# Kernel tuning notes

Measured on AMD Instinct MI355X. Metric: run time of the kernel, lower is better.

The kernel has to match this reference:

```python
import jax, jax.numpy as jnp
import numpy as np

P = 4            # capsule pose side
D = P * P        # capsule dim = 16
N_CLASSES = 10
N_ROUT = 3


def squash(s, axis=-1):
    sq = (s ** 2).sum(axis=axis, keepdims=True)
    scale = sq / (1.0 + sq)
    return scale * s / jnp.sqrt(sq)


def setup_inputs() -> dict:
    key = jax.random.key(0)
    k1, k2, k3 = jax.random.split(key, 3)
    N, C, W, H = 32, 32, 16, 16
    l = jax.random.normal(k1, (N, C, D, W, H), dtype=jnp.float32)
    g = jax.random.normal(k2, (N, N_CLASSES, D), dtype=jnp.float32)
    weight = jax.random.normal(k3, (1, C, 1, N_CLASSES, P, P), dtype=jnp.float32)
    return {"l": l, "g": g, "weight": weight}


def reference(l, g, weight):
    N, C, Dd, W, H = l.shape
    K = N_CLASSES
    # (N, C, D, W, H) -> (N, C, W*H, P, P)
    lr = jnp.transpose(l, (0, 1, 3, 4, 2)).reshape(N, C, W * H, P, P)
    w = weight.reshape(C, K, P, P)
    # votes: broadcasted small matmul over (N, C, WH, K)
    V = jnp.einsum('ncwij,ckjl->ncwkil', lr, w)          # (N, C, WH, K, P, P)
    V = V.reshape(N, 1, 1, C * W * H, K, Dd)             # (N,1,1,B,K,D)
    gb = g[:, None, None, None, :, :]                    # (N,1,1,1,K,D)
    b = (gb * V).sum(axis=-1, keepdims=True)             # (N,1,1,B,K,1)
    # dynamic routing, iters = N_ROUT
    for i in range(N_ROUT):
        c = jax.nn.softmax(b, axis=4)
        v = squash((c * V).sum(axis=3, keepdims=True))   # (N,1,1,1,K,D)
        if i != N_ROUT - 1:
            b = b + (V * v).sum(axis=-1, keepdims=True)
    a = jax.nn.sigmoid(jnp.linalg.norm(v, axis=-1))      # (N,1,1,1,K)
    v = v.reshape(N, K, Dd)
    a = a.reshape(N, K)
    return (a, v)
```

## Files before the change

### kernel.cpp

```cpp
#include <hip/hip_runtime.h>
#include <math.h>

#define NB 32
#define CB 32
#define KC 10
#define PAD_LRT 260
#define PAD_TP  168


__device__ __forceinline__ float squash_term(const float* __restrict__ sp, int n, int tid) {
    const float* p = sp + (size_t)n * (CB * 160) + tid;
    float t0 = 0.f, t1 = 0.f, t2 = 0.f, t3 = 0.f;
    #pragma unroll
    for (int cc = 0; cc < 32; cc += 4) {
        t0 += p[cc * 160];       t1 += p[(cc + 1) * 160];
        t2 += p[(cc + 2) * 160]; t3 += p[(cc + 3) * 160];
    }
    float ssum = (t0 + t1) + (t2 + t3);
    float sq = ssum * ssum;
    sq += __shfl_xor(sq, 1, 16);
    sq += __shfl_xor(sq, 2, 16);
    sq += __shfl_xor(sq, 4, 16);
    sq += __shfl_xor(sq, 8, 16);
    sq = fmaxf(sq, 1e-30f);
    return ssum * sq / ((1.f + sq) * sqrtf(sq));
}

__device__ __forceinline__ void softmax_c(const float lr[16], const float* __restrict__ E,
                                          float* __restrict__ c_out, int tid) {
    float b[KC];
    #pragma unroll
    for (int k = 0; k < KC; ++k) {
        const float4* e4 = (const float4*)(E + k * 16);
        float4 e0 = e4[0], e1 = e4[1], e2 = e4[2], e3 = e4[3];
        float acc = 0.f;
        acc = fmaf(lr[0], e0.x, acc);  acc = fmaf(lr[1], e0.y, acc);
        acc = fmaf(lr[2], e0.z, acc);  acc = fmaf(lr[3], e0.w, acc);
        acc = fmaf(lr[4], e1.x, acc);  acc = fmaf(lr[5], e1.y, acc);
        acc = fmaf(lr[6], e1.z, acc);  acc = fmaf(lr[7], e1.w, acc);
        acc = fmaf(lr[8], e2.x, acc);  acc = fmaf(lr[9], e2.y, acc);
        acc = fmaf(lr[10], e2.z, acc); acc = fmaf(lr[11], e2.w, acc);
        acc = fmaf(lr[12], e3.x, acc); acc = fmaf(lr[13], e3.y, acc);
        acc = fmaf(lr[14], e3.z, acc); acc = fmaf(lr[15], e3.w, acc);
        b[k] = acc;
    }
    float mx = b[0];
    #pragma unroll
    for (int k = 1; k < KC; ++k) mx = fmaxf(mx, b[k]);
    float sum = 0.f;
    #pragma unroll
    for (int k = 0; k < KC; ++k) { b[k] = __expf(b[k] - mx); sum += b[k]; }
    const float inv = 1.f / sum;
    #pragma unroll
    for (int k = 0; k < KC; ++k) c_out[k * 256 + tid] = b[k] * inv;
}

__device__ __forceinline__ void tp_stage(const float* __restrict__ lrTp,
                                         const float* __restrict__ cl,
                                         float* __restrict__ Tp, int tid) {
    const int mg  = tid >> 4;
    const int r   = tid & 15;
    const int ija = r & 7;
    const int ijb = ija + 8;
    const int k0  = (r >> 3) * 5;
    const float4* lp0 = (const float4*)(lrTp + ija * PAD_LRT + mg * 16);
    const float4* lp1 = (const float4*)(lrTp + ijb * PAD_LRT + mg * 16);
    float4 a0 = lp0[0], a1 = lp0[1], a2 = lp0[2], a3 = lp0[3];
    float4 b0 = lp1[0], b1 = lp1[1], b2 = lp1[2], b3 = lp1[3];
    #pragma unroll
    for (int kk = 0; kk < 5; ++kk) {
        const int k = k0 + kk;
        const float4* cp = (const float4*)(cl + k * 256 + mg * 16);
        float4 c0 = cp[0], c1 = cp[1], c2 = cp[2], c3 = cp[3];
        float t0 = 0.f, t1 = 0.f;
        t0 = fmaf(c0.x, a0.x, t0); t1 = fmaf(c0.x, b0.x, t1);
        t0 = fmaf(c0.y, a0.y, t0); t1 = fmaf(c0.y, b0.y, t1);
        t0 = fmaf(c0.z, a0.z, t0); t1 = fmaf(c0.z, b0.z, t1);
        t0 = fmaf(c0.w, a0.w, t0); t1 = fmaf(c0.w, b0.w, t1);
        t0 = fmaf(c1.x, a1.x, t0); t1 = fmaf(c1.x, b1.x, t1);
        t0 = fmaf(c1.y, a1.y, t0); t1 = fmaf(c1.y, b1.y, t1);
        t0 = fmaf(c1.z, a1.z, t0); t1 = fmaf(c1.z, b1.z, t1);
        t0 = fmaf(c1.w, a1.w, t0); t1 = fmaf(c1.w, b1.w, t1);
        t0 = fmaf(c2.x, a2.x, t0); t1 = fmaf(c2.x, b2.x, t1);
        t0 = fmaf(c2.y, a2.y, t0); t1 = fmaf(c2.y, b2.y, t1);
        t0 = fmaf(c2.z, a2.z, t0); t1 = fmaf(c2.z, b2.z, t1);
        t0 = fmaf(c2.w, a2.w, t0); t1 = fmaf(c2.w, b2.w, t1);
        t0 = fmaf(c3.x, a3.x, t0); t1 = fmaf(c3.x, b3.x, t1);
        t0 = fmaf(c3.y, a3.y, t0); t1 = fmaf(c3.y, b3.y, t1);
        t0 = fmaf(c3.z, a3.z, t0); t1 = fmaf(c3.z, b3.z, t1);
        t0 = fmaf(c3.w, a3.w, t0); t1 = fmaf(c3.w, b3.w, t1);
        Tp[mg * PAD_TP + k * 16 + ija] = t0;
        Tp[mg * PAD_TP + k * 16 + ijb] = t1;
    }
}

__device__ __forceinline__ void t_reduce(const float* __restrict__ Tp,
                                         float* __restrict__ T, int tid) {
    if (tid < 160) {
        float t = 0.f;
        #pragma unroll
        for (int mg = 0; mg < 16; ++mg) t += Tp[mg * PAD_TP + tid];
        T[tid] = t;
    }
}

__device__ __forceinline__ void s_write(const float* __restrict__ T,
                                        const float* __restrict__ w,
                                        float* __restrict__ s_base, int tid) {
    if (tid < 160) {
        const int k = tid >> 4;
        const int i = (tid >> 2) & 3;
        const int le = tid & 3;
        const float4 t4 = *(const float4*)(T + k * 16 + i * 4);
        float sv = 0.f;
        sv = fmaf(t4.x, w[k * 16 + 0 + le], sv);
        sv = fmaf(t4.y, w[k * 16 + 4 + le], sv);
        sv = fmaf(t4.z, w[k * 16 + 8 + le], sv);
        sv = fmaf(t4.w, w[k * 16 + 12 + le], sv);
        s_base[tid] = sv;
    }
}

__global__ __launch_bounds__(256) void caps_main(
    const float* __restrict__ l, const float* __restrict__ g,
    const float* __restrict__ weight,
    const float* __restrict__ sp0, const float* __restrict__ sp1,
    float* __restrict__ s_out, int nv)
{
    __shared__ __align__(16) float w_lds[160];
    __shared__ __align__(16) float aeff_lds[160];
    __shared__ __align__(16) float E_lds[160];
    __shared__ __align__(16) float lrT[16 * PAD_LRT];
    __shared__ __align__(16) float c_lds[KC * 256];
    __shared__ __align__(16) float Tp[16 * PAD_TP];
    __shared__ __align__(16) float T_lds[160];

    const int tid = threadIdx.x;
    const int n = blockIdx.x >> 5;
    const int c = blockIdx.x & 31;

    if (tid < 160) w_lds[tid] = weight[c * 160 + tid];

    float lr[16];
    const float* lbase = l + (size_t)(n * CB + c) * 4096 + tid;
    #pragma unroll
    for (int ij = 0; ij < 16; ++ij) lr[ij] = lbase[ij * 256];
    #pragma unroll
    for (int ij = 0; ij < 16; ++ij) lrT[ij * PAD_LRT + tid] = lr[ij];

    if (tid < 160) {
        float a = g[n * 160 + tid];
        if (nv > 0) a += squash_term(sp0, n, tid);
        if (nv > 1) a += squash_term(sp1, n, tid);
        aeff_lds[tid] = a;
    }
    __syncthreads();

    if (tid < 160) {
        const int k = tid >> 4, i = (tid >> 2) & 3, j = tid & 3;
        const float4 a4 = *(const float4*)(aeff_lds + k * 16 + i * 4);
        const float4 w4 = *(const float4*)(w_lds + k * 16 + j * 4);
        E_lds[tid] = a4.x * w4.x + a4.y * w4.y + a4.z * w4.z + a4.w * w4.w;
    }
    __syncthreads();

    softmax_c(lr, E_lds, c_lds, tid);
    __syncthreads();
    tp_stage(lrT, c_lds, Tp, tid);
    __syncthreads();
    t_reduce(Tp, T_lds, tid);
    __syncthreads();
    s_write(T_lds, w_lds, s_out + (size_t)blockIdx.x * 160, tid);
}

__global__ __launch_bounds__(256) void caps_final(
    const float* __restrict__ sp2, float* __restrict__ out)
{
    const int idx = blockIdx.x * 256 + threadIdx.x;
    const int nk = idx >> 4;
    const int d = idx & 15;
    const int n = nk / 10;
    const int k = nk - n * 10;
    const float* sp = sp2 + (size_t)n * (CB * 160) + k * 16 + d;
    float t0 = 0.f, t1 = 0.f, t2 = 0.f, t3 = 0.f;
    #pragma unroll
    for (int cc = 0; cc < 32; cc += 4) {
        t0 += sp[cc * 160];       t1 += sp[(cc + 1) * 160];
        t2 += sp[(cc + 2) * 160]; t3 += sp[(cc + 3) * 160];
    }
    float ssum = (t0 + t1) + (t2 + t3);
    float sq = ssum * ssum;
    sq += __shfl_xor(sq, 1, 16);
    sq += __shfl_xor(sq, 2, 16);
    sq += __shfl_xor(sq, 4, 16);
    sq += __shfl_xor(sq, 8, 16);
    sq = fmaxf(sq, 1e-30f);
    out[320 + nk * 16 + d] = ssum * sq / ((1.f + sq) * sqrtf(sq));
    if (d == 0) {
        const float nrm = sq / (1.f + sq);
        out[nk] = 1.f / (1.f + __expf(-nrm));
    }
}

extern "C" void kernel_launch(void* const* d_in, const int* in_sizes, int n_in,
                              void* d_out, int out_size, void* d_ws, size_t ws_size,
                              hipStream_t stream) {
    const float* l = (const float*)d_in[0];
    const float* g = (const float*)d_in[1];
    const float* w = (const float*)d_in[2];
    float* out = (float*)d_out;
    float* ws = (float*)d_ws;

    float* s0 = ws;
    float* s1 = ws + 163840;
    float* s2 = ws + 327680;

    caps_main<<<dim3(NB * CB), dim3(256), 0, stream>>>(l, g, w, nullptr, nullptr, s0, 0);
    caps_main<<<dim3(NB * CB), dim3(256), 0, stream>>>(l, g, w, s0, nullptr, s1, 1);
    caps_main<<<dim3(NB * CB), dim3(256), 0, stream>>>(l, g, w, s0, s1, s2, 2);
    caps_final<<<dim3(20), dim3(256), 0, stream>>>(s2, out);
}
```

Baseline: 29.12 us.

## Fuse final squash into last routing pass via atomics and last-block counter

Removes the separate caps_final launch. In the last routing pass each block atomically adds its partial s into a per-sample sum, and a per-sample counter picks the last finishing block, which then computes squash and the sigmoid activation. The sum buffer and counters are zeroed inside the second pass. The global load of l is also moved after the g/squash prologue to overlap the two. This saves one launch and the 32-way reduction read, at the cost of atomic contention and a non-deterministic summation order.

```diff
diff --git a/kernel.cpp b/kernel.cpp
--- a/kernel.cpp
+++ b/kernel.cpp
@@ -104,28 +104,15 @@
     }
 }
 
-__device__ __forceinline__ void s_write(const float* __restrict__ T,
-                                        const float* __restrict__ w,
-                                        float* __restrict__ s_base, int tid) {
-    if (tid < 160) {
-        const int k = tid >> 4;
-        const int i = (tid >> 2) & 3;
-        const int le = tid & 3;
-        const float4 t4 = *(const float4*)(T + k * 16 + i * 4);
-        float sv = 0.f;
-        sv = fmaf(t4.x, w[k * 16 + 0 + le], sv);
-        sv = fmaf(t4.y, w[k * 16 + 4 + le], sv);
-        sv = fmaf(t4.z, w[k * 16 + 8 + le], sv);
-        sv = fmaf(t4.w, w[k * 16 + 12 + le], sv);
-        s_base[tid] = sv;
-    }
-}
-
 __global__ __launch_bounds__(256) void caps_main(
     const float* __restrict__ l, const float* __restrict__ g,
     const float* __restrict__ weight,
     const float* __restrict__ sp0, const float* __restrict__ sp1,
-    float* __restrict__ s_out, int nv)
+    float* __restrict__ s_out,
+    float* __restrict__ s2_sum,
+    int* __restrict__ ctr,
+    float* __restrict__ out,
+    int nv)
 {
     __shared__ __align__(16) float w_lds[160];
     __shared__ __align__(16) float aeff_lds[160];
@@ -134,19 +121,19 @@
     __shared__ __align__(16) float c_lds[KC * 256];
     __shared__ __align__(16) float Tp[16 * PAD_TP];
     __shared__ __align__(16) float T_lds[160];
+    __shared__ int lastflag;
 
     const int tid = threadIdx.x;
-    const int n = blockIdx.x >> 5;
-    const int c = blockIdx.x & 31;
+    const int bid = blockIdx.x;
+    const int n = bid >> 5;
+    const int c = bid & 31;
+
+    if (nv == 1) {
+        if (bid < 20) s2_sum[bid * 256 + tid] = 0.f;
+        else if (bid == 20 && tid < 32) ctr[tid] = 0;
+    }
 
     if (tid < 160) w_lds[tid] = weight[c * 160 + tid];
-
-    float lr[16];
-    const float* lbase = l + (size_t)(n * CB + c) * 4096 + tid;
-    #pragma unroll
-    for (int ij = 0; ij < 16; ++ij) lr[ij] = lbase[ij * 256];
-    #pragma unroll
-    for (int ij = 0; ij < 16; ++ij) lrT[ij * PAD_LRT + tid] = lr[ij];
 
     if (tid < 160) {
         float a = g[n * 160 + tid];
@@ -154,6 +141,13 @@
         if (nv > 1) a += squash_term(sp1, n, tid);
         aeff_lds[tid] = a;
     }
+
+    float lr[16];
+    const float* lbase = l + (size_t)bid * 4096 + tid;
+    #pragma unroll
+    for (int ij = 0; ij < 16; ++ij) lr[ij] = lbase[ij * 256];
+    #pragma unroll
+    for (int ij = 0; ij < 16; ++ij) lrT[ij * PAD_LRT + tid] = lr[ij];
     __syncthreads();
 
     if (tid < 160) {
@@ -170,35 +164,49 @@
     __syncthreads();
     t_reduce(Tp, T_lds, tid);
     __syncthreads();
-    s_write(T_lds, w_lds, s_out + (size_t)blockIdx.x * 160, tid);
-}
-
-__global__ __launch_bounds__(256) void caps_final(
-    const float* __restrict__ sp2, float* __restrict__ out)
-{
-    const int idx = blockIdx.x * 256 + threadIdx.x;
-    const int nk = idx >> 4;
-    const int d = idx & 15;
-    const int n = nk / 10;
-    const int k = nk - n * 10;
-    const float* sp = sp2 + (size_t)n * (CB * 160) + k * 16 + d;
-    float t0 = 0.f, t1 = 0.f, t2 = 0.f, t3 = 0.f;
-    #pragma unroll
-    for (int cc = 0; cc < 32; cc += 4) {
-        t0 += sp[cc * 160];       t1 += sp[(cc + 1) * 160];
-        t2 += sp[(cc + 2) * 160]; t3 += sp[(cc + 3) * 160];
-    }
-    float ssum = (t0 + t1) + (t2 + t3);
-    float sq = ssum * ssum;
-    sq += __shfl_xor(sq, 1, 16);
-    sq += __shfl_xor(sq, 2, 16);
-    sq += __shfl_xor(sq, 4, 16);
-    sq += __shfl_xor(sq, 8, 16);
-    sq = fmaxf(sq, 1e-30f);
-    out[320 + nk * 16 + d] = ssum * sq / ((1.f + sq) * sqrtf(sq));
-    if (d == 0) {
-        const float nrm = sq / (1.f + sq);
-        out[nk] = 1.f / (1.f + __expf(-nrm));
+
+    if (tid < 160) {
+        const int k = tid >> 4;
+        const int i = (tid >> 2) & 3;
+        const int le = tid & 3;
+        const float4 t4 = *(const float4*)(T_lds + k * 16 + i * 4);
+        float sv = 0.f;
+        sv = fmaf(t4.x, w_lds[k * 16 + 0 + le], sv);
+        sv = fmaf(t4.y, w_lds[k * 16 + 4 + le], sv);
+        sv = fmaf(t4.z, w_lds[k * 16 + 8 + le], sv);
+        sv = fmaf(t4.w, w_lds[k * 16 + 12 + le], sv);
+        if (nv < 2) {
+            s_out[(size_t)bid * 160 + tid] = sv;
+        } else {
+            atomicAdd(&s2_sum[n * 160 + tid], sv);
+        }
+    }
+
+    if (nv != 2) return;
+
+    __syncthreads();
+    if (tid == 0) {
+        asm volatile("s_waitcnt vmcnt(0)" ::: "memory");
+        lastflag = (atomicAdd(&ctr[n], 1) == CB - 1);
+    }
+    __syncthreads();
+    if (!lastflag) return;
+
+    if (tid < 160) {
+        const float ssum = __hip_atomic_load(&s2_sum[n * 160 + tid],
+                                             __ATOMIC_RELAXED, __HIP_MEMORY_SCOPE_AGENT);
+        float sq = ssum * ssum;
+        sq += __shfl_xor(sq, 1, 16);
+        sq += __shfl_xor(sq, 2, 16);
+        sq += __shfl_xor(sq, 4, 16);
+        sq += __shfl_xor(sq, 8, 16);
+        sq = fmaxf(sq, 1e-30f);
+        const int k = tid >> 4, d = tid & 15;
+        out[320 + (n * KC + k) * 16 + d] = ssum * sq / ((1.f + sq) * sqrtf(sq));
+        if (d == 0) {
+            const float nrm = sq / (1.f + sq);
+            out[n * KC + k] = 1.f / (1.f + __expf(-nrm));
+        }
     }
 }
 
@@ -211,12 +219,15 @@
     float* out = (float*)d_out;
     float* ws = (float*)d_ws;
 
-    float* s0 = ws;
-    float* s1 = ws + 163840;
-    float* s2 = ws + 327680;
-
-    caps_main<<<dim3(NB * CB), dim3(256), 0, stream>>>(l, g, w, nullptr, nullptr, s0, 0);
-    caps_main<<<dim3(NB * CB), dim3(256), 0, stream>>>(l, g, w, s0, nullptr, s1, 1);
-    caps_main<<<dim3(NB * CB), dim3(256), 0, stream>>>(l, g, w, s0, s1, s2, 2);
-    caps_final<<<dim3(20), dim3(256), 0, stream>>>(s2, out);
-}
+    float* s0     = ws;
+    float* s1     = ws + 163840;
+    float* s2_sum = ws + 327680;
+    int*   ctr    = (int*)(ws + 332800);
+
+    caps_main<<<dim3(NB * CB), dim3(256), 0, stream>>>(
+        l, g, w, nullptr, nullptr, s0, s2_sum, ctr, out, 0);
+    caps_main<<<dim3(NB * CB), dim3(256), 0, stream>>>(
+        l, g, w, s0, nullptr, s1, s2_sum, ctr, out, 1);
+    caps_main<<<dim3(NB * CB), dim3(256), 0, stream>>>(
+        l, g, w, s0, s1, nullptr, s2_sum, ctr, out, 2);
+}
```

After: 35.98 us. +23.5%, slower.

## Double threads per block, split class work across thread pairs, fuse reduction stages

Applied to the files above, without the earlier changes.

Blocks grow from 256 to 512 threads. Each pair of threads shares one spatial position and splits the ten classes, combining the softmax max and sum with a lane shuffle. The two squash-term reductions run in parallel on separate thread groups, and the T reduction is folded into the final weight multiply so one barrier and one shared buffer go away. The aim is more parallelism and shorter per-thread serial chains in a latency-bound kernel. In exchange, every global load of l is issued twice, and more threads per block may reduce how many blocks fit on a CU.

```diff
diff --git a/kernel.cpp b/kernel.cpp
--- a/kernel.cpp
+++ b/kernel.cpp
@@ -8,8 +8,8 @@
 #define PAD_TP  168
 
 
-__device__ __forceinline__ float squash_term(const float* __restrict__ sp, int n, int tid) {
-    const float* p = sp + (size_t)n * (CB * 160) + tid;
+__device__ __forceinline__ float squash_term(const float* __restrict__ sp, int n, int t) {
+    const float* p = sp + (size_t)n * (CB * 160) + t;
     float t0 = 0.f, t1 = 0.f, t2 = 0.f, t3 = 0.f;
     #pragma unroll
     for (int cc = 0; cc < 32; cc += 4) {
@@ -26,151 +26,136 @@
     return ssum * sq / ((1.f + sq) * sqrtf(sq));
 }
 
-__device__ __forceinline__ void softmax_c(const float lr[16], const float* __restrict__ E,
-                                          float* __restrict__ c_out, int tid) {
-    float b[KC];
-    #pragma unroll
-    for (int k = 0; k < KC; ++k) {
-        const float4* e4 = (const float4*)(E + k * 16);
-        float4 e0 = e4[0], e1 = e4[1], e2 = e4[2], e3 = e4[3];
-        float acc = 0.f;
-        acc = fmaf(lr[0], e0.x, acc);  acc = fmaf(lr[1], e0.y, acc);
-        acc = fmaf(lr[2], e0.z, acc);  acc = fmaf(lr[3], e0.w, acc);
-        acc = fmaf(lr[4], e1.x, acc);  acc = fmaf(lr[5], e1.y, acc);
-        acc = fmaf(lr[6], e1.z, acc);  acc = fmaf(lr[7], e1.w, acc);
-        acc = fmaf(lr[8], e2.x, acc);  acc = fmaf(lr[9], e2.y, acc);
-        acc = fmaf(lr[10], e2.z, acc); acc = fmaf(lr[11], e2.w, acc);
-        acc = fmaf(lr[12], e3.x, acc); acc = fmaf(lr[13], e3.y, acc);
-        acc = fmaf(lr[14], e3.z, acc); acc = fmaf(lr[15], e3.w, acc);
-        b[k] = acc;
-    }
-    float mx = b[0];
-    #pragma unroll
-    for (int k = 1; k < KC; ++k) mx = fmaxf(mx, b[k]);
-    float sum = 0.f;
-    #pragma unroll
-    for (int k = 0; k < KC; ++k) { b[k] = __expf(b[k] - mx); sum += b[k]; }
-    const float inv = 1.f / sum;
-    #pragma unroll
-    for (int k = 0; k < KC; ++k) c_out[k * 256 + tid] = b[k] * inv;
-}
-
-__device__ __forceinline__ void tp_stage(const float* __restrict__ lrTp,
-                                         const float* __restrict__ cl,
-                                         float* __restrict__ Tp, int tid) {
-    const int mg  = tid >> 4;
-    const int r   = tid & 15;
-    const int ija = r & 7;
-    const int ijb = ija + 8;
-    const int k0  = (r >> 3) * 5;
-    const float4* lp0 = (const float4*)(lrTp + ija * PAD_LRT + mg * 16);
-    const float4* lp1 = (const float4*)(lrTp + ijb * PAD_LRT + mg * 16);
-    float4 a0 = lp0[0], a1 = lp0[1], a2 = lp0[2], a3 = lp0[3];
-    float4 b0 = lp1[0], b1 = lp1[1], b2 = lp1[2], b3 = lp1[3];
-    #pragma unroll
-    for (int kk = 0; kk < 5; ++kk) {
-        const int k = k0 + kk;
-        const float4* cp = (const float4*)(cl + k * 256 + mg * 16);
-        float4 c0 = cp[0], c1 = cp[1], c2 = cp[2], c3 = cp[3];
-        float t0 = 0.f, t1 = 0.f;
-        t0 = fmaf(c0.x, a0.x, t0); t1 = fmaf(c0.x, b0.x, t1);
-        t0 = fmaf(c0.y, a0.y, t0); t1 = fmaf(c0.y, b0.y, t1);
-        t0 = fmaf(c0.z, a0.z, t0); t1 = fmaf(c0.z, b0.z, t1);
-        t0 = fmaf(c0.w, a0.w, t0); t1 = fmaf(c0.w, b0.w, t1);
-        t0 = fmaf(c1.x, a1.x, t0); t1 = fmaf(c1.x, b1.x, t1);
-        t0 = fmaf(c1.y, a1.y, t0); t1 = fmaf(c1.y, b1.y, t1);
-        t0 = fmaf(c1.z, a1.z, t0); t1 = fmaf(c1.z, b1.z, t1);
-        t0 = fmaf(c1.w, a1.w, t0); t1 = fmaf(c1.w, b1.w, t1);
-        t0 = fmaf(c2.x, a2.x, t0); t1 = fmaf(c2.x, b2.x, t1);
-        t0 = fmaf(c2.y, a2.y, t0); t1 = fmaf(c2.y, b2.y, t1);
-        t0 = fmaf(c2.z, a2.z, t0); t1 = fmaf(c2.z, b2.z, t1);
-        t0 = fmaf(c2.w, a2.w, t0); t1 = fmaf(c2.w, b2.w, t1);
-        t0 = fmaf(c3.x, a3.x, t0); t1 = fmaf(c3.x, b3.x, t1);
-        t0 = fmaf(c3.y, a3.y, t0); t1 = fmaf(c3.y, b3.y, t1);
-        t0 = fmaf(c3.z, a3.z, t0); t1 = fmaf(c3.z, b3.z, t1);
-        t0 = fmaf(c3.w, a3.w, t0); t1 = fmaf(c3.w, b3.w, t1);
-        Tp[mg * PAD_TP + k * 16 + ija] = t0;
-        Tp[mg * PAD_TP + k * 16 + ijb] = t1;
-    }
-}
-
-__device__ __forceinline__ void t_reduce(const float* __restrict__ Tp,
-                                         float* __restrict__ T, int tid) {
-    if (tid < 160) {
-        float t = 0.f;
-        #pragma unroll
-        for (int mg = 0; mg < 16; ++mg) t += Tp[mg * PAD_TP + tid];
-        T[tid] = t;
-    }
-}
-
-__device__ __forceinline__ void s_write(const float* __restrict__ T,
-                                        const float* __restrict__ w,
-                                        float* __restrict__ s_base, int tid) {
-    if (tid < 160) {
-        const int k = tid >> 4;
-        const int i = (tid >> 2) & 3;
-        const int le = tid & 3;
-        const float4 t4 = *(const float4*)(T + k * 16 + i * 4);
-        float sv = 0.f;
-        sv = fmaf(t4.x, w[k * 16 + 0 + le], sv);
-        sv = fmaf(t4.y, w[k * 16 + 4 + le], sv);
-        sv = fmaf(t4.z, w[k * 16 + 8 + le], sv);
-        sv = fmaf(t4.w, w[k * 16 + 12 + le], sv);
-        s_base[tid] = sv;
-    }
-}
-
-__global__ __launch_bounds__(256) void caps_main(
+__global__ __launch_bounds__(512, 8) void caps_main(
     const float* __restrict__ l, const float* __restrict__ g,
     const float* __restrict__ weight,
     const float* __restrict__ sp0, const float* __restrict__ sp1,
     float* __restrict__ s_out, int nv)
 {
     __shared__ __align__(16) float w_lds[160];
-    __shared__ __align__(16) float aeff_lds[160];
+    __shared__ __align__(16) float aeffA[160];
+    __shared__ __align__(16) float aeffB[160];
     __shared__ __align__(16) float E_lds[160];
     __shared__ __align__(16) float lrT[16 * PAD_LRT];
     __shared__ __align__(16) float c_lds[KC * 256];
     __shared__ __align__(16) float Tp[16 * PAD_TP];
-    __shared__ __align__(16) float T_lds[160];
 
     const int tid = threadIdx.x;
-    const int n = blockIdx.x >> 5;
-    const int c = blockIdx.x & 31;
-
-    if (tid < 160) w_lds[tid] = weight[c * 160 + tid];
-
-    float lr[16];
-    const float* lbase = l + (size_t)(n * CB + c) * 4096 + tid;
-    #pragma unroll
-    for (int ij = 0; ij < 16; ++ij) lr[ij] = lbase[ij * 256];
-    #pragma unroll
-    for (int ij = 0; ij < 16; ++ij) lrT[ij * PAD_LRT + tid] = lr[ij];
+    const int bid = blockIdx.x;
+    const int n = bid >> 5;
+    const int c = bid & 31;
 
     if (tid < 160) {
         float a = g[n * 160 + tid];
         if (nv > 0) a += squash_term(sp0, n, tid);
-        if (nv > 1) a += squash_term(sp1, n, tid);
-        aeff_lds[tid] = a;
+        aeffA[tid] = a;
+        w_lds[tid] = weight[c * 160 + tid];
+    } else if (tid >= 256 && tid < 416) {
+        const int t = tid - 256;
+        aeffB[t] = (nv > 1) ? squash_term(sp1, n, t) : 0.f;
+    }
+
+    const int m  = tid >> 1;
+    const int kh = tid & 1;
+    float lr[16];
+    {
+        const float* lbase = l + (size_t)bid * 4096 + m;
+        #pragma unroll
+        for (int ij = 0; ij < 16; ++ij) lr[ij] = lbase[ij * 256];
+        if (kh == 0) {
+            #pragma unroll
+            for (int ij = 0; ij < 16; ++ij) lrT[ij * PAD_LRT + m] = lr[ij];
+        }
     }
     __syncthreads();
 
     if (tid < 160) {
         const int k = tid >> 4, i = (tid >> 2) & 3, j = tid & 3;
-        const float4 a4 = *(const float4*)(aeff_lds + k * 16 + i * 4);
+        const float4 a4 = *(const float4*)(aeffA + k * 16 + i * 4);
+        const float4 b4 = *(const float4*)(aeffB + k * 16 + i * 4);
         const float4 w4 = *(const float4*)(w_lds + k * 16 + j * 4);
-        E_lds[tid] = a4.x * w4.x + a4.y * w4.y + a4.z * w4.z + a4.w * w4.w;
-    }
-    __syncthreads();
-
-    softmax_c(lr, E_lds, c_lds, tid);
-    __syncthreads();
-    tp_stage(lrT, c_lds, Tp, tid);
-    __syncthreads();
-    t_reduce(Tp, T_lds, tid);
-    __syncthreads();
-    s_write(T_lds, w_lds, s_out + (size_t)blockIdx.x * 160, tid);
+        E_lds[tid] = (a4.x + b4.x) * w4.x + (a4.y + b4.y) * w4.y
+                   + (a4.z + b4.z) * w4.z + (a4.w + b4.w) * w4.w;
+    }
+    __syncthreads();
+
+    {
+        float b[5];
+        #pragma unroll
+        for (int kk = 0; kk < 5; ++kk) {
+            const int k = kh * 5 + kk;
+            const float4* e4 = (const float4*)(E_lds + k * 16);
+            float4 e0 = e4[0], e1 = e4[1], e2 = e4[2], e3 = e4[3];
+            float acc = 0.f;
+            acc = fmaf(lr[0], e0.x, acc);  acc = fmaf(lr[1], e0.y, acc);
+            acc = fmaf(lr[2], e0.z, acc);  acc = fmaf(lr[3], e0.w, acc);
+            acc = fmaf(lr[4], e1.x, acc);  acc = fmaf(lr[5], e1.y, acc);
+            acc = fmaf(lr[6], e1.z, acc);  acc = fmaf(lr[7], e1.w, acc);
+            acc = fmaf(lr[8], e2.x, acc);  acc = fmaf(lr[9], e2.y, acc);
+            acc = fmaf(lr[10], e2.z, acc); acc = fmaf(lr[11], e2.w, acc);
+            acc = fmaf(lr[12], e3.x, acc); acc = fmaf(lr[13], e3.y, acc);
+            acc = fmaf(lr[14], e3.z, acc); acc = fmaf(lr[15], e3.w, acc);
+            b[kk] = acc;
+        }
+        float mx = b[0];
+        #pragma unroll
+        for (int kk = 1; kk < 5; ++kk) mx = fmaxf(mx, b[kk]);
+        mx = fmaxf(mx, __shfl_xor(mx, 1, 64));
+        float sum = 0.f;
+        #pragma unroll
+        for (int kk = 0; kk < 5; ++kk) { b[kk] = __expf(b[kk] - mx); sum += b[kk]; }
+        sum += __shfl_xor(sum, 1, 64);
+        const float inv = 1.f / sum;
+        #pragma unroll
+        for (int kk = 0; kk < 5; ++kk)
+            c_lds[(kh * 5 + kk) * 256 + m] = b[kk] * inv;
+    }
+    __syncthreads();
+
+    {
+        const int mg  = tid >> 5;
+        const int ij  = (tid >> 1) & 15;
+        const int kh2 = tid & 1;
+        const float4* lp = (const float4*)(lrT + ij * PAD_LRT + mg * 16);
+        float4 a0 = lp[0], a1 = lp[1], a2 = lp[2], a3 = lp[3];
+        #pragma unroll
+        for (int kk = 0; kk < 5; ++kk) {
+            const int k = kh2 * 5 + kk;
+            const float4* cp = (const float4*)(c_lds + k * 256 + mg * 16);
+            float4 c0 = cp[0], c1 = cp[1], c2 = cp[2], c3 = cp[3];
+            float t = 0.f;
+            t = fmaf(c0.x, a0.x, t); t = fmaf(c0.y, a0.y, t);
+            t = fmaf(c0.z, a0.z, t); t = fmaf(c0.w, a0.w, t);
+            t = fmaf(c1.x, a1.x, t); t = fmaf(c1.y, a1.y, t);
+            t = fmaf(c1.z, a1.z, t); t = fmaf(c1.w, a1.w, t);
+            t = fmaf(c2.x, a2.x, t); t = fmaf(c2.y, a2.y, t);
+            t = fmaf(c2.z, a2.z, t); t = fmaf(c2.w, a2.w, t);
+            t = fmaf(c3.x, a3.x, t); t = fmaf(c3.y, a3.y, t);
+            t = fmaf(c3.w, a3.w, t); t = fmaf(c3.z, a3.z, t);
+            Tp[mg * PAD_TP + k * 16 + ij] = t;
+        }
+    }
+    __syncthreads();
+
+    if (tid < 160) {
+        const int k = tid >> 4;
+        const int i = (tid >> 2) & 3;
+        const int le = tid & 3;
+        const float w0 = w_lds[k * 16 + 0  + le];
+        const float w1 = w_lds[k * 16 + 4  + le];
+        const float w2 = w_lds[k * 16 + 8  + le];
+        const float w3 = w_lds[k * 16 + 12 + le];
+        float sv = 0.f;
+        #pragma unroll
+        for (int mg = 0; mg < 16; ++mg) {
+            const float4 t4 = *(const float4*)(Tp + mg * PAD_TP + k * 16 + i * 4);
+            sv = fmaf(t4.x, w0, sv);
+            sv = fmaf(t4.y, w1, sv);
+            sv = fmaf(t4.z, w2, sv);
+            sv = fmaf(t4.w, w3, sv);
+        }
+        s_out[(size_t)bid * 160 + tid] = sv;
+    }
 }
 
 __global__ __launch_bounds__(256) void caps_final(
@@ -215,8 +200,8 @@
     float* s1 = ws + 163840;
     float* s2 = ws + 327680;
 
-    caps_main<<<dim3(NB * CB), dim3(256), 0, stream>>>(l, g, w, nullptr, nullptr, s0, 0);
-    caps_main<<<dim3(NB * CB), dim3(256), 0, stream>>>(l, g, w, s0, nullptr, s1, 1);
-    caps_main<<<dim3(NB * CB), dim3(256), 0, stream>>>(l, g, w, s0, s1, s2, 2);
+    caps_main<<<dim3(NB * CB), dim3(512), 0, stream>>>(l, g, w, nullptr, nullptr, s0, 0);
+    caps_main<<<dim3(NB * CB), dim3(512), 0, stream>>>(l, g, w, s0, nullptr, s1, 1);
+    caps_main<<<dim3(NB * CB), dim3(512), 0, stream>>>(l, g, w, s0, s1, s2, 2);
     caps_final<<<dim3(20), dim3(256), 0, stream>>>(s2, out);
 }
```

After: 33.99 us. +16.7%, slower.
